# Kernel optimization log

Hardware: AMD Instinct MI355X
Metric: run time of the kernel (lower is better)

Reference implementation:

```python
import jax, jax.numpy as jnp
import numpy as np

DIM = 1024

def setup_inputs() -> dict:
    key = jax.random.key(0)
    ks = jax.random.split(key, 7)
    s = 1.0 / np.sqrt(DIM)
    x = jax.random.normal(ks[0], (8, 2048, DIM), dtype=jnp.float32)
    Wq = jax.random.uniform(ks[1], (DIM, DIM), jnp.float32, -s, s)
    bq = jax.random.uniform(ks[2], (DIM,), jnp.float32, -s, s)
    Wk = jax.random.uniform(ks[3], (DIM, DIM), jnp.float32, -s, s)
    bk = jax.random.uniform(ks[4], (DIM,), jnp.float32, -s, s)
    Wv = jax.random.uniform(ks[5], (DIM, DIM), jnp.float32, -s, s)
    bv = jax.random.uniform(ks[6], (DIM,), jnp.float32, -s, s)
    return {"x": x, "Wq": Wq, "bq": bq, "Wk": Wk, "bk": bk, "Wv": Wv, "bv": bv}

def reference(x, Wq, bq, Wk, bk, Wv, bv):
    # x: [B, S, D]; torch Linear: x @ W.T + b (W here stored transposed: [D_in, D_out])
    scale = x.shape[-1] ** (-0.5)
    q = x @ Wq + bq                      # [B, S, D]
    k = x @ Wk + bk
    v = x @ Wv + bv
    scores = jnp.einsum('bsd,btd->bst', q, k) * scale  # [B, S, S]
    attn = jax.nn.softmax(scores, axis=-1)
    out = jnp.einsum('bst,btd->bsd', attn, v)          # [B, S, D]
    return out.mean(axis=1)                            # [B, D]
```

## Files before the change

### kernel.cpp

```cpp
#include <hip/hip_runtime.h>


using bf16x8 = __attribute__((ext_vector_type(8))) __bf16;
using u16x8  = __attribute__((ext_vector_type(8))) unsigned short;
using f32x4  = __attribute__((ext_vector_type(4))) float;
using f32x2  = __attribute__((ext_vector_type(2))) float;

#define NB 8
#define SEQ 2048
#define DIM 1024
#define MTOT (NB * SEQ)

__device__ __forceinline__ unsigned short f2bf(float f) {
    unsigned int u = __float_as_uint(f);
    u = u + 0x7FFFu + ((u >> 16) & 1u);
    return (unsigned short)(u >> 16);
}
__device__ __forceinline__ float bf2f(unsigned short h) {
    return __uint_as_float(((unsigned int)h) << 16);
}

__device__ __forceinline__ void async16(const unsigned short* g, unsigned short* l) {
    __builtin_amdgcn_global_load_lds(
        (const __attribute__((address_space(1))) void*)g,
        (__attribute__((address_space(3))) void*)l, 16, 0, 0);
}

__global__ __launch_bounds__(256) void k_prep(const float* __restrict__ Wk,
                                              const float* __restrict__ Wq,
                                              const float* __restrict__ bq,
                                              const float* __restrict__ bv,
                                              unsigned short* __restrict__ wkb,
                                              unsigned short* __restrict__ wqb,
                                              float* __restrict__ u,
                                              float* __restrict__ out) {
    const int bid = blockIdx.x;
    if (bid < 2048) {
        const float* src = (bid >= 1024) ? Wq : Wk;
        unsigned short* dst = (bid >= 1024) ? wqb : wkb;
        size_t i = ((size_t)(bid & 1023) * 256 + threadIdx.x) * 4;
        float4 v = *reinterpret_cast<const float4*>(src + i);
        ushort4 o;
        o.x = f2bf(v.x); o.y = f2bf(v.y); o.z = f2bf(v.z); o.w = f2bf(v.w);
        *reinterpret_cast<ushort4*>(dst + i) = o;
    } else if (bid < 2304) {
        const int wave = threadIdx.x >> 6, lane = threadIdx.x & 63;
        const int row = (bid - 2048) * 4 + wave;
        const float* wr = Wk + (size_t)row * DIM;
        float s = 0.f;
#pragma unroll
        for (int p = 0; p < 4; ++p) {
            int col = p * 256 + lane * 4;
            float4 v = *reinterpret_cast<const float4*>(wr + col);
            float4 b = *reinterpret_cast<const float4*>(bq + col);
            s += v.x * b.x + v.y * b.y + v.z * b.z + v.w * b.w;
        }
#pragma unroll
        for (int off = 32; off; off >>= 1) s += __shfl_xor(s, off);
        if (lane == 0) u[row] = s;
    } else {
        int i = (bid - 2304) * 256 + threadIdx.x;
        out[i] = bv[i & (DIM - 1)];
    }
}

__global__ __launch_bounds__(256) void k_cvt_x(const float* __restrict__ x,
                                               const float* __restrict__ u,
                                               unsigned short* __restrict__ xb,
                                               float* __restrict__ c) {
    __shared__ float red[4];
    const int row = blockIdx.x, tid = threadIdx.x;
    size_t i = (size_t)row * DIM + tid * 4;
    float4 v = *reinterpret_cast<const float4*>(x + i);
    ushort4 o;
    o.x = f2bf(v.x); o.y = f2bf(v.y); o.z = f2bf(v.z); o.w = f2bf(v.w);
    *reinterpret_cast<ushort4*>(xb + i) = o;
    float4 uv = *reinterpret_cast<const float4*>(u + tid * 4);
    float s = v.x * uv.x + v.y * uv.y + v.z * uv.z + v.w * uv.w;
#pragma unroll
    for (int off = 32; off; off >>= 1) s += __shfl_xor(s, off);
    if ((tid & 63) == 0) red[tid >> 6] = s;
    __syncthreads();
    if (tid == 0) c[row] = 0.03125f * (red[0] + red[1] + red[2] + red[3]);
}

__device__ __forceinline__ void gemm_bt_tile128(const unsigned short* __restrict__ A,
                                                const unsigned short* __restrict__ Bt,
                                                int K, int m0, int n0, int lda, int ldb,
                                                unsigned short* ldsA, unsigned short* ldsB,
                                                f32x4 acc[4][4]) {
    const int tid  = threadIdx.x;
    const int wave = tid >> 6;
    const int lane = tid & 63;
    const int lrow = lane >> 3;
    const int lcol = lane & 7;
    const int wm = (wave >> 1) * 64;
    const int wn = (wave & 1) * 64;
    const int fr = lane & 15;
    const int fg = lane >> 4;

    for (int k0 = 0; k0 < K; k0 += 64) {
#pragma unroll
        for (int r = 0; r < 4; ++r) {
            int row = r * 32 + wave * 8 + lrow;
            async16(A + (size_t)(m0 + row) * lda + k0 + lcol * 8, ldsA + r * 2048 + wave * 512);
            async16(Bt + (size_t)(n0 + row) * ldb + k0 + lcol * 8, ldsB + r * 2048 + wave * 512);
        }
        __syncthreads();
#pragma unroll
        for (int ks = 0; ks < 2; ++ks) {
            bf16x8 af[4], bfr[4];
#pragma unroll
            for (int mf = 0; mf < 4; ++mf)
                af[mf] = *reinterpret_cast<const bf16x8*>(ldsA + (wm + mf * 16 + fr) * 64 + ks * 32 + fg * 8);
#pragma unroll
            for (int nf = 0; nf < 4; ++nf)
                bfr[nf] = *reinterpret_cast<const bf16x8*>(ldsB + (wn + nf * 16 + fr) * 64 + ks * 32 + fg * 8);
#pragma unroll
            for (int mf = 0; mf < 4; ++mf)
#pragma unroll
                for (int nf = 0; nf < 4; ++nf)
                    acc[mf][nf] = __builtin_amdgcn_mfma_f32_16x16x32_bf16(af[mf], bfr[nf], acc[mf][nf], 0, 0, 0);
        }
        __syncthreads();
    }
}

__global__ __launch_bounds__(256) void k_mm(const unsigned short* __restrict__ wkb,
                                            const unsigned short* __restrict__ wqb,
                                            unsigned short* __restrict__ Mt) {
    __shared__ unsigned short ldsA[128 * 64];
    __shared__ unsigned short ldsB[128 * 64];
    int m0 = blockIdx.x * 128, n0 = blockIdx.y * 128;
    f32x4 acc[4][4] = {};
    gemm_bt_tile128(wkb, wqb, DIM, m0, n0, DIM, DIM, ldsA, ldsB, acc);
    const int lane = threadIdx.x & 63, wave = threadIdx.x >> 6;
    const int wm = (wave >> 1) * 64, wn = (wave & 1) * 64;
    const int fr = lane & 15, fg = lane >> 4;
#pragma unroll
    for (int nf = 0; nf < 4; ++nf) {
        int n = n0 + wn + nf * 16 + fr;
#pragma unroll
        for (int mf = 0; mf < 4; ++mf) {
            int r0 = m0 + wm + mf * 16 + fg * 4;
#pragma unroll
            for (int j = 0; j < 4; ++j)
                Mt[(size_t)(r0 + j) * DIM + n] = f2bf(acc[mf][nf][j]);
        }
    }
}


#define STAGE(gbase, ld, dstoff)                                          \
    do {                                                                  \
        async16((gbase), ldsw + (dstoff));                                \
        async16((gbase) + 8 * (size_t)(ld), ldsw + (dstoff) + 512);       \
    } while (0)
#define STAGE_A(buf, half, kt) STAGE(gA + (size_t)((half) * 128) * lda + (kt) * 64, lda, (buf) * 16384 + (half) * 8192)
#define STAGE_B(buf, half, kt) STAGE(gB + (size_t)((half) * 128) * ldb + (kt) * 64, ldb, 32768 + (buf) * 16384 + (half) * 8192)

#define FRAG(base_us, row, colb) \
    (*(const bf16x8*)((const char*)(lds + (base_us)) + (row) * 128 + ((colb) ^ (((row) & 7) << 4))))

#define READ_A(dbuf, mh)                                                      \
    _Pragma("unroll") for (int m2 = 0; m2 < 4; ++m2) {                        \
        int arow = ((mh) * 4 + m2) * 16 + fr;                                 \
        _Pragma("unroll") for (int ks = 0; ks < 2; ++ks)                      \
            afc[(mh) * 4 + m2][ks] =                                          \
                FRAG((dbuf) * 16384 + wr * 8192, arow, ks * 64 + fg * 16);    \
    }
#define READ_B(dbuf, nh)                                                      \
    _Pragma("unroll") for (int n2 = 0; n2 < 2; ++n2) {                        \
        int brow = (wc & 1) * 64 + ((nh) * 2 + n2) * 16 + fr;                 \
        _Pragma("unroll") for (int ks = 0; ks < 2; ++ks)                      \
            bfc[nh][n2][ks] =                                                 \
                FRAG(32768 + (dbuf) * 16384 + (wc >> 1) * 8192, brow,         \
                     ks * 64 + fg * 16);                                      \
    }

#define VM4 asm volatile("s_waitcnt vmcnt(4)" ::: "memory")

#define PHASE(mh, nh, STG, VM, PF)                                            \
    do {                                                                      \
        STG;                                                                  \
        VM;                                                                   \
        asm volatile("s_barrier" ::: "memory");                               \
        asm volatile("s_waitcnt lgkmcnt(0)" ::: "memory");                    \
        __builtin_amdgcn_sched_barrier(0);                                    \
        PF;                                                                   \
        __builtin_amdgcn_sched_barrier(0);                                    \
        __builtin_amdgcn_s_setprio(1);                                        \
        _Pragma("unroll") for (int m2 = 0; m2 < 4; ++m2)                      \
            _Pragma("unroll") for (int n2 = 0; n2 < 2; ++n2) {                \
                f32x4& a = acc[(mh) * 4 + m2][(nh) * 2 + n2];                 \
                a = __builtin_amdgcn_mfma_f32_16x16x32_bf16(                  \
                    afc[(mh) * 4 + m2][0], bfc[nh][n2][0], a, 0, 0, 0);       \
                a = __builtin_amdgcn_mfma_f32_16x16x32_bf16(                  \
                    afc[(mh) * 4 + m2][1], bfc[nh][n2][1], a, 0, 0, 0);       \
            }                                                                 \
        __builtin_amdgcn_s_setprio(0);                                        \
    } while (0)

__device__ __forceinline__ void gemm256(const unsigned short* __restrict__ A,
                                        const unsigned short* __restrict__ Bt,
                                        int lda, int ldb, int m0, int n0,
                                        unsigned short* lds, f32x4 (&acc)[8][4]) {
    constexpr int NKT = 1024 / 64;
    constexpr int NIT = NKT / 2;
    const int tid = threadIdx.x;
    const int w = tid >> 6, lane = tid & 63;
    const int wr = w >> 2, wc = w & 3;
    const int fr = lane & 15, fg = lane >> 4;
    const int r8 = lane >> 3, slot = (lane & 7) ^ r8;

    const unsigned short* gA = A + (size_t)(m0 + w * 16 + r8) * lda + slot * 8;
    const unsigned short* gB = Bt + (size_t)(n0 + w * 16 + r8) * ldb + slot * 8;
    unsigned short* ldsw = lds + w * 1024;

    bf16x8 afc[8][2];
    bf16x8 bfc[2][2][2];

    STAGE_A(0, 0, 0); STAGE_A(0, 1, 0); STAGE_B(0, 0, 0); STAGE_B(0, 1, 0);
    STAGE_A(1, 0, 1); STAGE_A(1, 1, 1);
    VM4;
    asm volatile("s_barrier" ::: "memory");
    READ_A(0, 0); READ_B(0, 0);

    for (int it = 0; it < NIT; ++it) {
        const int t1 = 2 * it + 1;
        const int ka = (2 * it + 2) & (NKT - 1);
        const int kb = (2 * it + 3) & (NKT - 1);
        PHASE(0, 0, STAGE_B(1, 0, t1), , READ_A(0, 1));
        PHASE(1, 0, STAGE_B(1, 1, t1), , READ_B(0, 1));
        PHASE(0, 1, STAGE_A(0, 0, ka), , );
        PHASE(1, 1, STAGE_A(0, 1, ka), VM4, READ_A(1, 0); READ_B(1, 0));
        PHASE(0, 0, STAGE_B(0, 0, ka), , READ_A(1, 1));
        PHASE(1, 0, STAGE_B(0, 1, ka), , READ_B(1, 1));
        PHASE(0, 1, STAGE_A(1, 0, kb), , );
        PHASE(1, 1, STAGE_A(1, 1, kb), VM4, READ_A(0, 0); READ_B(0, 0));
    }
    asm volatile("s_waitcnt vmcnt(0) lgkmcnt(0)" ::: "memory");
}

__global__ __launch_bounds__(512, 2) void k_proj_y(const unsigned short* __restrict__ xb,
                                                   const unsigned short* __restrict__ Mt,
                                                   unsigned short* __restrict__ y) {
    __shared__ unsigned short lds[65536];
    const int f = blockIdx.x;
    const int m_hi = f & 7, j = f >> 3;
    const int n_t = j & 3, m_lo = j >> 2;
    const int m0 = (m_hi * 8 + m_lo) * 256, n0 = n_t * 256;

    f32x4 acc[8][4] = {};
    gemm256(xb, Mt, DIM, DIM, m0, n0, lds, acc);

    const int tid = threadIdx.x, w = tid >> 6, lane = tid & 63;
    const int wr = w >> 2, wc = w & 3, fr = lane & 15, fg = lane >> 4;
#pragma unroll
    for (int nf = 0; nf < 4; ++nf) {
        int n = n0 + wc * 64 + nf * 16 + fr;
#pragma unroll
        for (int mf = 0; mf < 8; ++mf) {
            int r0 = m0 + wr * 128 + mf * 16 + fg * 4;
#pragma unroll
            for (int j2 = 0; j2 < 4; ++j2)
                y[(size_t)(r0 + j2) * DIM + n] = f2bf(acc[mf][nf][j2]);
        }
    }
}

__global__ __launch_bounds__(512, 2) void k_scores(const unsigned short* __restrict__ y,
                                                   const unsigned short* __restrict__ xb,
                                                   const float* __restrict__ c,
                                                   unsigned char* __restrict__ PT,
                                                   float* __restrict__ ell) {
    __shared__ unsigned short lds[65536];
    const int f = blockIdx.x;
    const int b = f & 7, j = f >> 3;
    const int mt = j & 7, nt = j >> 3;
    const unsigned short* q = y + (size_t)b * SEQ * DIM;
    const unsigned short* k = xb + (size_t)b * SEQ * DIM;
    const int m0 = mt * 256, n0 = nt * 256;

    f32x4 acc[8][4] = {};
    gemm256(q, k, DIM, DIM, m0, n0, lds, acc);

    const float scl = 0.03125f;
    const int tid = threadIdx.x, w = tid >> 6, lane = tid & 63;
    const int wr = w >> 2, wc = w & 3, fr = lane & 15, fg = lane >> 4;
    unsigned char* Pb = PT + (size_t)b * SEQ * SEQ;
    float cv[4];
#pragma unroll
    for (int nf = 0; nf < 4; ++nf)
        cv[nf] = c[(size_t)b * SEQ + n0 + wc * 64 + nf * 16 + fr];
#pragma unroll
    for (int mf = 0; mf < 8; ++mf) {
        const int sbase = m0 + wr * 128 + mf * 16 + fg * 4;
        float rs[4] = {0.f, 0.f, 0.f, 0.f};
#pragma unroll
        for (int nf = 0; nf < 4; ++nf) {
            int t = n0 + wc * 64 + nf * 16 + fr;
            float p0 = __expf(fmaf(acc[mf][nf][0], scl, cv[nf]));
            float p1 = __expf(fmaf(acc[mf][nf][1], scl, cv[nf]));
            float p2 = __expf(fmaf(acc[mf][nf][2], scl, cv[nf]));
            float p3 = __expf(fmaf(acc[mf][nf][3], scl, cv[nf]));
            int pk = __builtin_amdgcn_cvt_pk_fp8_f32(p0, p1, 0, false);
            pk = __builtin_amdgcn_cvt_pk_fp8_f32(p2, p3, pk, true);
            *reinterpret_cast<unsigned int*>(Pb + (size_t)t * SEQ + sbase) = (unsigned int)pk;
            f32x2 d01 = __builtin_amdgcn_cvt_pk_f32_fp8(pk, false);
            f32x2 d23 = __builtin_amdgcn_cvt_pk_f32_fp8(pk, true);
            rs[0] += d01[0]; rs[1] += d01[1]; rs[2] += d23[0]; rs[3] += d23[1];
        }
#pragma unroll
        for (int j2 = 0; j2 < 4; ++j2) {
            float r = rs[j2];
            r += __shfl_xor(r, 1);
            r += __shfl_xor(r, 2);
            r += __shfl_xor(r, 4);
            r += __shfl_xor(r, 8);
            if (fr == 0) atomicAdd(&ell[b * SEQ + sbase + j2], r);
        }
    }
}

__global__ __launch_bounds__(256) void k_colsum(const unsigned char* __restrict__ PT,
                                                const float* __restrict__ ell,
                                                float* __restrict__ w) {
    __shared__ float rel[512];
    const int b = blockIdx.z;
    const int s0 = blockIdx.x * 512;
    const int t = blockIdx.y * 256 + threadIdx.x;
    {
        int i = threadIdx.x;
        rel[i]       = 1.0f / ell[b * SEQ + s0 + i];
        rel[i + 256] = 1.0f / ell[b * SEQ + s0 + 256 + i];
    }
    __syncthreads();
    const unsigned char* Pt = PT + (size_t)b * SEQ * SEQ + (size_t)t * SEQ + s0;
    float a = 0.f;
    for (int i = 0; i < 512; i += 8) {
        uint2 pv = *reinterpret_cast<const uint2*>(Pt + i);
        f32x2 d0 = __builtin_amdgcn_cvt_pk_f32_fp8((int)pv.x, false);
        f32x2 d1 = __builtin_amdgcn_cvt_pk_f32_fp8((int)pv.x, true);
        f32x2 d2 = __builtin_amdgcn_cvt_pk_f32_fp8((int)pv.y, false);
        f32x2 d3 = __builtin_amdgcn_cvt_pk_f32_fp8((int)pv.y, true);
        a += d0[0] * rel[i]     + d0[1] * rel[i + 1] + d1[0] * rel[i + 2] + d1[1] * rel[i + 3];
        a += d2[0] * rel[i + 4] + d2[1] * rel[i + 5] + d3[0] * rel[i + 6] + d3[1] * rel[i + 7];
    }
    atomicAdd(&w[b * SEQ + t], a);
}

__global__ __launch_bounds__(256) void k_accx(const float* __restrict__ w,
                                              const unsigned short* __restrict__ xb,
                                              float* __restrict__ g) {
    const int b = blockIdx.y;
    const int t0 = blockIdx.x * 64 + (threadIdx.x >> 7) * 32;
    const int d8 = (threadIdx.x & 127) * 8;
    const unsigned short* xbb = xb + (size_t)b * SEQ * DIM;
    const float* wb = w + b * SEQ;
    float a[8] = {};
    for (int i = 0; i < 32; ++i) {
        int t = t0 + i;
        float wt = wb[t];
        u16x8 v = *reinterpret_cast<const u16x8*>(xbb + (size_t)t * DIM + d8);
#pragma unroll
        for (int j = 0; j < 8; ++j) a[j] += wt * bf2f(v[j]);
    }
#pragma unroll
    for (int j = 0; j < 8; ++j)
        atomicAdd(&g[b * DIM + d8 + j], a[j] * (1.0f / (float)SEQ));
}

__global__ __launch_bounds__(256) void k_out2(const float* __restrict__ g,
                                              const float* __restrict__ Wv,
                                              float* __restrict__ out) {
    int b = blockIdx.y;
    int n = blockIdx.x * 256 + threadIdx.x;
    int d0 = blockIdx.z * 64;
    const float* gb = g + b * DIM;
    float acc = 0.f;
#pragma unroll
    for (int d = 0; d < 64; ++d)
        acc += gb[d0 + d] * Wv[(size_t)(d0 + d) * DIM + n];
    atomicAdd(&out[b * DIM + n], acc);
}

extern "C" void kernel_launch(void* const* d_in, const int* in_sizes, int n_in,
                              void* d_out, int out_size, void* d_ws, size_t ws_size,
                              hipStream_t stream) {
    const float* x  = (const float*)d_in[0];
    const float* Wq = (const float*)d_in[1];
    const float* bq = (const float*)d_in[2];
    const float* Wk = (const float*)d_in[3];
    const float* bk = (const float*)d_in[4];
    const float* Wv = (const float*)d_in[5];
    const float* bv = (const float*)d_in[6];
    float* out = (float*)d_out;
    (void)bk;

    char* ws = (char*)d_ws;
    unsigned short* xb  = (unsigned short*)(ws);
    unsigned short* wkb = (unsigned short*)(ws + 33554432ull);
    unsigned short* wqb = (unsigned short*)(ws + 35651584ull);
    unsigned short* Mt  = (unsigned short*)(ws + 37748736ull);
    unsigned short* y   = (unsigned short*)(ws + 39845888ull);
    unsigned char*  PT  = (unsigned char*)(ws + 73400320ull);
    float*          ell = (float*)(ws + 106954752ull);
    float*          w   = (float*)(ws + 107020288ull);
    float*          g   = (float*)(ws + 107085824ull);
    float*          c   = (float*)(ws + 107118592ull);
    float*          u   = (float*)(ws + 107184128ull);

    hipMemsetAsync(ell, 0, 163840, stream);

    k_prep<<<dim3(2336), 256, 0, stream>>>(Wk, Wq, bq, bv, wkb, wqb, u, out);
    k_cvt_x<<<dim3(MTOT), 256, 0, stream>>>(x, u, xb, c);
    k_mm<<<dim3(8, 8), 256, 0, stream>>>(wkb, wqb, Mt);
    k_proj_y<<<dim3(256), 512, 0, stream>>>(xb, Mt, y);
    k_scores<<<dim3(512), 512, 0, stream>>>(y, xb, c, PT, ell);
    k_colsum<<<dim3(SEQ / 512, SEQ / 256, NB), 256, 0, stream>>>(PT, ell, w);
    k_accx<<<dim3(SEQ / 64, NB), 256, 0, stream>>>(w, xb, g);
    k_out2<<<dim3(DIM / 256, NB, 16), 256, 0, stream>>>(g, Wv, out);
}
```

Before: 206.6 us.

## Switch projection and score GEMMs from bf16 to fp8 MFMA with scaled operands

Adds fp8 copies of x, M and y, and rewrites the 256x256 GEMM pipeline to stage fp8 tiles (K=128 per stage) and use 16x16x32 fp8 MFMAs in both k_proj_y and k_scores. M is stored scaled by 64 and y by 1/8, and the score scale is adjusted to compensate. The aim is to halve operand bytes and LDS traffic per K-step and to use the higher fp8 matrix throughput. The cost is lower numerical precision in scores, an extra fp8 store of x in k_cvt_x (the bf16 copy of x is kept for k_accx), and less headroom for overflow in the scaled operands.

After: 214.1 us. +3.6%, slower.

```diff
diff --git a/kernel.cpp b/kernel.cpp
--- a/kernel.cpp
+++ b/kernel.cpp
@@ -21,6 +21,11 @@
 }
 
 __device__ __forceinline__ void async16(const unsigned short* g, unsigned short* l) {
+    __builtin_amdgcn_global_load_lds(
+        (const __attribute__((address_space(1))) void*)g,
+        (__attribute__((address_space(3))) void*)l, 16, 0, 0);
+}
+__device__ __forceinline__ void async16b(const unsigned char* g, unsigned char* l) {
     __builtin_amdgcn_global_load_lds(
         (const __attribute__((address_space(1))) void*)g,
         (__attribute__((address_space(3))) void*)l, 16, 0, 0);
@@ -67,6 +72,7 @@
 __global__ __launch_bounds__(256) void k_cvt_x(const float* __restrict__ x,
                                                const float* __restrict__ u,
                                                unsigned short* __restrict__ xb,
+                                               unsigned char* __restrict__ xb8,
                                                float* __restrict__ c) {
     __shared__ float red[4];
     const int row = blockIdx.x, tid = threadIdx.x;
@@ -75,6 +81,9 @@
     ushort4 o;
     o.x = f2bf(v.x); o.y = f2bf(v.y); o.z = f2bf(v.z); o.w = f2bf(v.w);
     *reinterpret_cast<ushort4*>(xb + i) = o;
+    int pk = __builtin_amdgcn_cvt_pk_fp8_f32(v.x, v.y, 0, false);
+    pk = __builtin_amdgcn_cvt_pk_fp8_f32(v.z, v.w, pk, true);
+    *reinterpret_cast<unsigned int*>(xb8 + i) = (unsigned int)pk;
     float4 uv = *reinterpret_cast<const float4*>(u + tid * 4);
     float s = v.x * uv.x + v.y * uv.y + v.z * uv.z + v.w * uv.w;
 #pragma unroll
@@ -128,7 +137,7 @@
 
 __global__ __launch_bounds__(256) void k_mm(const unsigned short* __restrict__ wkb,
                                             const unsigned short* __restrict__ wqb,
-                                            unsigned short* __restrict__ Mt) {
+                                            unsigned char* __restrict__ Mt8) {
     __shared__ unsigned short ldsA[128 * 64];
     __shared__ unsigned short ldsB[128 * 64];
     int m0 = blockIdx.x * 128, n0 = blockIdx.y * 128;
@@ -143,44 +152,47 @@
 #pragma unroll
         for (int mf = 0; mf < 4; ++mf) {
             int r0 = m0 + wm + mf * 16 + fg * 4;
-#pragma unroll
-            for (int j = 0; j < 4; ++j)
-                Mt[(size_t)(r0 + j) * DIM + n] = f2bf(acc[mf][nf][j]);
-        }
-    }
-}
-
-
-#define STAGE(gbase, ld, dstoff)                                          \
+            int pk01 = __builtin_amdgcn_cvt_pk_fp8_f32(acc[mf][nf][0] * 64.f, acc[mf][nf][1] * 64.f, 0, false);
+            int pk23 = __builtin_amdgcn_cvt_pk_fp8_f32(acc[mf][nf][2] * 64.f, acc[mf][nf][3] * 64.f, 0, false);
+            Mt8[(size_t)(r0 + 0) * DIM + n] = (unsigned char)(pk01 & 0xff);
+            Mt8[(size_t)(r0 + 1) * DIM + n] = (unsigned char)((pk01 >> 8) & 0xff);
+            Mt8[(size_t)(r0 + 2) * DIM + n] = (unsigned char)(pk23 & 0xff);
+            Mt8[(size_t)(r0 + 3) * DIM + n] = (unsigned char)((pk23 >> 8) & 0xff);
+        }
+    }
+}
+
+
+#define STAGE8(gbase, ld, dstoff)                                         \
     do {                                                                  \
-        async16((gbase), ldsw + (dstoff));                                \
-        async16((gbase) + 8 * (size_t)(ld), ldsw + (dstoff) + 512);       \
+        async16b((gbase), ldsb + (dstoff));                               \
+        async16b((gbase) + 8 * (size_t)(ld), ldsb + (dstoff) + 1024);     \
     } while (0)
-#define STAGE_A(buf, half, kt) STAGE(gA + (size_t)((half) * 128) * lda + (kt) * 64, lda, (buf) * 16384 + (half) * 8192)
-#define STAGE_B(buf, half, kt) STAGE(gB + (size_t)((half) * 128) * ldb + (kt) * 64, ldb, 32768 + (buf) * 16384 + (half) * 8192)
-
-#define FRAG(base_us, row, colb) \
-    (*(const bf16x8*)((const char*)(lds + (base_us)) + (row) * 128 + ((colb) ^ (((row) & 7) << 4))))
-
-#define READ_A(dbuf, mh)                                                      \
+#define STAGE8_A(buf, half, kt) STAGE8(gA + (size_t)((half) * 128) * lda + (kt) * 128, lda, (buf) * 32768 + (half) * 16384)
+#define STAGE8_B(buf, half, kt) STAGE8(gB + (size_t)((half) * 128) * ldb + (kt) * 128, ldb, 65536 + (buf) * 32768 + (half) * 16384)
+
+#define FRAG8(base_b, row, colb) \
+    (*reinterpret_cast<const long*>(ldsb + (base_b) + (row) * 128 + ((colb) ^ (((row) & 7) << 4))))
+
+#define READ8_A(dbuf, mh)                                                     \
     _Pragma("unroll") for (int m2 = 0; m2 < 4; ++m2) {                        \
         int arow = ((mh) * 4 + m2) * 16 + fr;                                 \
-        _Pragma("unroll") for (int ks = 0; ks < 2; ++ks)                      \
+        _Pragma("unroll") for (int ks = 0; ks < 4; ++ks)                      \
             afc[(mh) * 4 + m2][ks] =                                          \
-                FRAG((dbuf) * 16384 + wr * 8192, arow, ks * 64 + fg * 16);    \
-    }
-#define READ_B(dbuf, nh)                                                      \
+                FRAG8((dbuf) * 32768 + wr * 16384, arow, ks * 32 + fg * 8);   \
+    }
+#define READ8_B(dbuf, nh)                                                     \
     _Pragma("unroll") for (int n2 = 0; n2 < 2; ++n2) {                        \
         int brow = (wc & 1) * 64 + ((nh) * 2 + n2) * 16 + fr;                 \
-        _Pragma("unroll") for (int ks = 0; ks < 2; ++ks)                      \
+        _Pragma("unroll") for (int ks = 0; ks < 4; ++ks)                      \
             bfc[nh][n2][ks] =                                                 \
-                FRAG(32768 + (dbuf) * 16384 + (wc >> 1) * 8192, brow,         \
-                     ks * 64 + fg * 16);                                      \
+                FRAG8(65536 + (dbuf) * 32768 + (wc >> 1) * 16384, brow,       \
+                      ks * 32 + fg * 8);                                      \
     }
 
 #define VM4 asm volatile("s_waitcnt vmcnt(4)" ::: "memory")
 
-#define PHASE(mh, nh, STG, VM, PF)                                            \
+#define PHASE8(mh, nh, STG, VM, PF)                                           \
     do {                                                                      \
         STG;                                                                  \
         VM;                                                                   \
@@ -191,21 +203,20 @@
         __builtin_amdgcn_sched_barrier(0);                                    \
         __builtin_amdgcn_s_setprio(1);                                        \
         _Pragma("unroll") for (int m2 = 0; m2 < 4; ++m2)                      \
-            _Pragma("unroll") for (int n2 = 0; n2 < 2; ++n2) {                \
-                f32x4& a = acc[(mh) * 4 + m2][(nh) * 2 + n2];                 \
-                a = __builtin_amdgcn_mfma_f32_16x16x32_bf16(                  \
-                    afc[(mh) * 4 + m2][0], bfc[nh][n2][0], a, 0, 0, 0);       \
-                a = __builtin_amdgcn_mfma_f32_16x16x32_bf16(                  \
-                    afc[(mh) * 4 + m2][1], bfc[nh][n2][1], a, 0, 0, 0);       \
-            }                                                                 \
+        _Pragma("unroll") for (int n2 = 0; n2 < 2; ++n2)                      \
+        _Pragma("unroll") for (int ks = 0; ks < 4; ++ks)                      \
+            acc[(mh) * 4 + m2][(nh) * 2 + n2] =                               \
+                __builtin_amdgcn_mfma_f32_16x16x32_fp8_fp8(                   \
+                    afc[(mh) * 4 + m2][ks], bfc[nh][n2][ks],                  \
+                    acc[(mh) * 4 + m2][(nh) * 2 + n2], 0, 0, 0);              \
         __builtin_amdgcn_s_setprio(0);                                        \
     } while (0)
 
-__device__ __forceinline__ void gemm256(const unsigned short* __restrict__ A,
-                                        const unsigned short* __restrict__ Bt,
-                                        int lda, int ldb, int m0, int n0,
-                                        unsigned short* lds, f32x4 (&acc)[8][4]) {
-    constexpr int NKT = 1024 / 64;
+__device__ __forceinline__ void gemm256_fp8(const unsigned char* __restrict__ A,
+                                            const unsigned char* __restrict__ Bt,
+                                            int lda, int ldb, int m0, int n0,
+                                            unsigned char* ldsb, f32x4 (&acc)[8][4]) {
+    constexpr int NKT = 1024 / 128;
     constexpr int NIT = NKT / 2;
     const int tid = threadIdx.x;
     const int w = tid >> 6, lane = tid & 63;
@@ -213,46 +224,61 @@
     const int fr = lane & 15, fg = lane >> 4;
     const int r8 = lane >> 3, slot = (lane & 7) ^ r8;
 
-    const unsigned short* gA = A + (size_t)(m0 + w * 16 + r8) * lda + slot * 8;
-    const unsigned short* gB = Bt + (size_t)(n0 + w * 16 + r8) * ldb + slot * 8;
-    unsigned short* ldsw = lds + w * 1024;
-
-    bf16x8 afc[8][2];
-    bf16x8 bfc[2][2][2];
-
-    STAGE_A(0, 0, 0); STAGE_A(0, 1, 0); STAGE_B(0, 0, 0); STAGE_B(0, 1, 0);
-    STAGE_A(1, 0, 1); STAGE_A(1, 1, 1);
+    const unsigned char* gA = A + (size_t)(m0 + w * 16 + r8) * lda + slot * 16;
+    const unsigned char* gB = Bt + (size_t)(n0 + w * 16 + r8) * ldb + slot * 16;
+    unsigned char* ldsbw = ldsb + w * 2048;
+    #define ldsb ldsbw_alias
+    unsigned char* ldsbw_alias = ldsbw;
+    #undef ldsb
+
+    long afc[8][4];
+    long bfc[2][2][4];
+
+    {
+        unsigned char* ldsb = ldsbw;
+        STAGE8_A(0, 0, 0); STAGE8_A(0, 1, 0); STAGE8_B(0, 0, 0); STAGE8_B(0, 1, 0);
+        STAGE8_A(1, 0, 1); STAGE8_A(1, 1, 1);
+    }
     VM4;
     asm volatile("s_barrier" ::: "memory");
-    READ_A(0, 0); READ_B(0, 0);
-
+    {
+        unsigned char* ldsb = ldsbw - w * 2048;
+        READ8_A(0, 0); READ8_B(0, 0);
+    }
+
+    unsigned char* ldsb_rd = ldsbw - w * 2048;
     for (int it = 0; it < NIT; ++it) {
         const int t1 = 2 * it + 1;
         const int ka = (2 * it + 2) & (NKT - 1);
         const int kb = (2 * it + 3) & (NKT - 1);
-        PHASE(0, 0, STAGE_B(1, 0, t1), , READ_A(0, 1));
-        PHASE(1, 0, STAGE_B(1, 1, t1), , READ_B(0, 1));
-        PHASE(0, 1, STAGE_A(0, 0, ka), , );
-        PHASE(1, 1, STAGE_A(0, 1, ka), VM4, READ_A(1, 0); READ_B(1, 0));
-        PHASE(0, 0, STAGE_B(0, 0, ka), , READ_A(1, 1));
-        PHASE(1, 0, STAGE_B(0, 1, ka), , READ_B(1, 1));
-        PHASE(0, 1, STAGE_A(1, 0, kb), , );
-        PHASE(1, 1, STAGE_A(1, 1, kb), VM4, READ_A(0, 0); READ_B(0, 0));
+        unsigned char* ldsb = ldsbw;
+        {
+            #define RD_LDS unsigned char* ldsb = ldsb_rd;
+            PHASE8(0, 0, STAGE8_B(1, 0, t1), , { RD_LDS READ8_A(0, 1); });
+            PHASE8(1, 0, STAGE8_B(1, 1, t1), , { RD_LDS READ8_B(0, 1); });
+            PHASE8(0, 1, STAGE8_A(0, 0, ka), , );
+            PHASE8(1, 1, STAGE8_A(0, 1, ka), VM4, { RD_LDS READ8_A(1, 0); READ8_B(1, 0); });
+            PHASE8(0, 0, STAGE8_B(0, 0, ka), , { RD_LDS READ8_A(1, 1); });
+            PHASE8(1, 0, STAGE8_B(0, 1, ka), , { RD_LDS READ8_B(1, 1); });
+            PHASE8(0, 1, STAGE8_A(1, 0, kb), , );
+            PHASE8(1, 1, STAGE8_A(1, 1, kb), VM4, { RD_LDS READ8_A(0, 0); READ8_B(0, 0); });
+            #undef RD_LDS
+        }
     }
     asm volatile("s_waitcnt vmcnt(0) lgkmcnt(0)" ::: "memory");
 }
 
-__global__ __launch_bounds__(512, 2) void k_proj_y(const unsigned short* __restrict__ xb,
-                                                   const unsigned short* __restrict__ Mt,
-                                                   unsigned short* __restrict__ y) {
-    __shared__ unsigned short lds[65536];
+__global__ __launch_bounds__(512, 2) void k_proj_y(const unsigned char* __restrict__ xb8,
+                                                   const unsigned char* __restrict__ Mt8,
+                                                   unsigned char* __restrict__ y8) {
+    __shared__ unsigned char lds[131072];
     const int f = blockIdx.x;
     const int m_hi = f & 7, j = f >> 3;
     const int n_t = j & 3, m_lo = j >> 2;
     const int m0 = (m_hi * 8 + m_lo) * 256, n0 = n_t * 256;
 
     f32x4 acc[8][4] = {};
-    gemm256(xb, Mt, DIM, DIM, m0, n0, lds, acc);
+    gemm256_fp8(xb8, Mt8, DIM, DIM, m0, n0, lds, acc);
 
     const int tid = threadIdx.x, w = tid >> 6, lane = tid & 63;
     const int wr = w >> 2, wc = w & 3, fr = lane & 15, fg = lane >> 4;
@@ -262,30 +288,33 @@
 #pragma unroll
         for (int mf = 0; mf < 8; ++mf) {
             int r0 = m0 + wr * 128 + mf * 16 + fg * 4;
-#pragma unroll
-            for (int j2 = 0; j2 < 4; ++j2)
-                y[(size_t)(r0 + j2) * DIM + n] = f2bf(acc[mf][nf][j2]);
-        }
-    }
-}
-
-__global__ __launch_bounds__(512, 2) void k_scores(const unsigned short* __restrict__ y,
-                                                   const unsigned short* __restrict__ xb,
+            int pk01 = __builtin_amdgcn_cvt_pk_fp8_f32(acc[mf][nf][0] * 0.125f, acc[mf][nf][1] * 0.125f, 0, false);
+            int pk23 = __builtin_amdgcn_cvt_pk_fp8_f32(acc[mf][nf][2] * 0.125f, acc[mf][nf][3] * 0.125f, 0, false);
+            y8[(size_t)(r0 + 0) * DIM + n] = (unsigned char)(pk01 & 0xff);
+            y8[(size_t)(r0 + 1) * DIM + n] = (unsigned char)((pk01 >> 8) & 0xff);
+            y8[(size_t)(r0 + 2) * DIM + n] = (unsigned char)(pk23 & 0xff);
+            y8[(size_t)(r0 + 3) * DIM + n] = (unsigned char)((pk23 >> 8) & 0xff);
+        }
+    }
+}
+
+__global__ __launch_bounds__(512, 2) void k_scores(const unsigned char* __restrict__ y8,
+                                                   const unsigned char* __restrict__ xb8,
                                                    const float* __restrict__ c,
                                                    unsigned char* __restrict__ PT,
                                                    float* __restrict__ ell) {
-    __shared__ unsigned short lds[65536];
+    __shared__ unsigned char lds[131072];
     const int f = blockIdx.x;
     const int b = f & 7, j = f >> 3;
     const int mt = j & 7, nt = j >> 3;
-    const unsigned short* q = y + (size_t)b * SEQ * DIM;
-    const unsigned short* k = xb + (size_t)b * SEQ * DIM;
+    const unsigned char* q = y8 + (size_t)b * SEQ * DIM;
+    const unsigned char* k = xb8 + (size_t)b * SEQ * DIM;
     const int m0 = mt * 256, n0 = nt * 256;
 
     f32x4 acc[8][4] = {};
-    gemm256(q, k, DIM, DIM, m0, n0, lds, acc);
-
-    const float scl = 0.03125f;
+    gemm256_fp8(q, k, DIM, DIM, m0, n0, lds, acc);
+
+    const float scl8 = 0.00390625f;
     const int tid = threadIdx.x, w = tid >> 6, lane = tid & 63;
     const int wr = w >> 2, wc = w & 3, fr = lane & 15, fg = lane >> 4;
     unsigned char* Pb = PT + (size_t)b * SEQ * SEQ;
@@ -300,10 +329,10 @@
 #pragma unroll
         for (int nf = 0; nf < 4; ++nf) {
             int t = n0 + wc * 64 + nf * 16 + fr;
-            float p0 = __expf(fmaf(acc[mf][nf][0], scl, cv[nf]));
-            float p1 = __expf(fmaf(acc[mf][nf][1], scl, cv[nf]));
-            float p2 = __expf(fmaf(acc[mf][nf][2], scl, cv[nf]));
-            float p3 = __expf(fmaf(acc[mf][nf][3], scl, cv[nf]));
+            float p0 = __expf(fmaf(acc[mf][nf][0], scl8, cv[nf]));
+            float p1 = __expf(fmaf(acc[mf][nf][1], scl8, cv[nf]));
+            float p2 = __expf(fmaf(acc[mf][nf][2], scl8, cv[nf]));
+            float p3 = __expf(fmaf(acc[mf][nf][3], scl8, cv[nf]));
             int pk = __builtin_amdgcn_cvt_pk_fp8_f32(p0, p1, 0, false);
             pk = __builtin_amdgcn_cvt_pk_fp8_f32(p2, p3, pk, true);
             *reinterpret_cast<unsigned int*>(Pb + (size_t)t * SEQ + sbase) = (unsigned int)pk;
@@ -402,22 +431,23 @@
     unsigned short* xb  = (unsigned short*)(ws);
     unsigned short* wkb = (unsigned short*)(ws + 33554432ull);
     unsigned short* wqb = (unsigned short*)(ws + 35651584ull);
-    unsigned short* Mt  = (unsigned short*)(ws + 37748736ull);
-    unsigned short* y   = (unsigned short*)(ws + 39845888ull);
-    unsigned char*  PT  = (unsigned char*)(ws + 73400320ull);
-    float*          ell = (float*)(ws + 106954752ull);
-    float*          w   = (float*)(ws + 107020288ull);
-    float*          g   = (float*)(ws + 107085824ull);
-    float*          c   = (float*)(ws + 107118592ull);
-    float*          u   = (float*)(ws + 107184128ull);
+    unsigned char*  Mt8 = (unsigned char*)(ws + 37748736ull);
+    unsigned char*  xb8 = (unsigned char*)(ws + 38797312ull);
+    unsigned char*  y8  = (unsigned char*)(ws + 55574528ull);
+    unsigned char*  PT  = (unsigned char*)(ws + 72351744ull);
+    float*          ell = (float*)(ws + 105906176ull);
+    float*          w   = (float*)(ws + 105971712ull);
+    float*          g   = (float*)(ws + 106037248ull);
+    float*          c   = (float*)(ws + 106070016ull);
+    float*          u   = (float*)(ws + 106135552ull);
 
     hipMemsetAsync(ell, 0, 163840, stream);
 
     k_prep<<<dim3(2336), 256, 0, stream>>>(Wk, Wq, bq, bv, wkb, wqb, u, out);
-    k_cvt_x<<<dim3(MTOT), 256, 0, stream>>>(x, u, xb, c);
-    k_mm<<<dim3(8, 8), 256, 0, stream>>>(wkb, wqb, Mt);
-    k_proj_y<<<dim3(256), 512, 0, stream>>>(xb, Mt, y);
-    k_scores<<<dim3(512), 512, 0, stream>>>(y, xb, c, PT, ell);
+    k_cvt_x<<<dim3(MTOT), 256, 0, stream>>>(x, u, xb, xb8, c);
+    k_mm<<<dim3(8, 8), 256, 0, stream>>>(wkb, wqb, Mt8);
+    k_proj_y<<<dim3(256), 512, 0, stream>>>(xb8, Mt8, y8);
+    k_scores<<<dim3(512), 512, 0, stream>>>(y8, xb8, c, PT, ell);
     k_colsum<<<dim3(SEQ / 512, SEQ / 256, NB), 256, 0, stream>>>(PT, ell, w);
     k_accx<<<dim3(SEQ / 64, NB), 256, 0, stream>>>(w, xb, g);
     k_out2<<<dim3(DIM / 256, NB, 16), 256, 0, stream>>>(g, Wv, out);
```
